# Optimization experiments

Measured on AMD Instinct MI355X. Metric: run time of the kernel, lower is better.

## Reference

```python
import jax, jax.numpy as jnp
import numpy as np

# Block sizes (DGL message-flow-graph / sampled blocks)
NS0, ND0, NE0 = 300000, 50000, 800000   # block0: 2-hop frontier -> 1-hop frontier
NS1, ND1, NE1 = 50000, 8192, 131072     # block1: 1-hop frontier -> seed nodes


def _graph_conv(x, src, dst, ew, W, b, n_src, n_dst, weight_first):
    """DGL GraphConv with norm='both' and edge_weight.

    x: [n_src, d_in] source-node features; (src, dst): edge endpoints;
    ew: [E] edge weights. Degrees are UNWEIGHTED (copy of DGL semantics),
    clamped to >= 1. Weight applied before aggregation iff d_in > d_out.
    """
    ones_e = jnp.ones_like(ew)
    out_deg = jnp.clip(jax.ops.segment_sum(ones_e, src, num_segments=n_src), 1.0, None)
    h = x * (out_deg ** -0.5)[:, None]
    if weight_first:
        h = h @ W
    # gather-weight-scatter: m_v = sum_{e: e->v} ew_e * h_{src_e}
    msg = jax.ops.segment_sum(ew[:, None] * h[src], dst, num_segments=n_dst)
    in_deg = jnp.clip(jax.ops.segment_sum(ones_e, dst, num_segments=n_dst), 1.0, None)
    msg = msg * (in_deg ** -0.5)[:, None]
    if not weight_first:
        msg = msg @ W
    return msg + b


def setup_inputs() -> dict:
    key = jax.random.key(0)
    ks = jax.random.split(key, 12)
    in_f, hid_f, out_f = 256, 128, 128
    return {
        "x": jax.random.normal(ks[0], (NS0, in_f), dtype=jnp.float32),
        "src0": jax.random.randint(ks[1], (NE0,), 0, NS0, dtype=jnp.int64 if jax.config.jax_enable_x64 else jnp.int32).astype(jnp.int32),
        "dst0": jax.random.randint(ks[2], (NE0,), 0, ND0).astype(jnp.int32),
        "ew0": jax.random.normal(ks[3], (NE0,), dtype=jnp.float32),
        "src1": jax.random.randint(ks[4], (NE1,), 0, NS1).astype(jnp.int32),
        "dst1": jax.random.randint(ks[5], (NE1,), 0, ND1).astype(jnp.int32),
        "ew1": jax.random.normal(ks[6], (NE1,), dtype=jnp.float32),
        "W1": jax.random.normal(ks[7], (in_f, hid_f), dtype=jnp.float32) * 0.05,
        "b1": jax.random.normal(ks[8], (hid_f,), dtype=jnp.float32) * 0.05,
        "W2": jax.random.normal(ks[9], (hid_f, out_f), dtype=jnp.float32) * 0.05,
        "b2": jax.random.normal(ks[10], (out_f,), dtype=jnp.float32) * 0.05,
    }


def reference(x, src0, dst0, ew0, src1, dst1, ew1, W1, b1, W2, b2):
    # layer 1: in(256) > hidden(128) -> weight applied before aggregation
    h = jax.nn.relu(_graph_conv(x, src0, dst0, ew0, W1, b1, NS0, ND0, weight_first=True))
    # layer 2: hidden(128) <= out(128) -> aggregate then weight
    out = jax.nn.relu(_graph_conv(h, src1, dst1, ew1, W2, b2, NS1, ND1, weight_first=False))
    return out  # [ND1, out_f]
```

## Files before the change

### kernel.cpp

```cpp
#include <hip/hip_runtime.h>

#define NS0 300000
#define ND0 50000
#define NE0 800000
#define NS1 50000
#define ND1 8192
#define NE1 131072
#define IN_F 256
#define HID_F 128
#define SLOTS 64
#define NTILE (NS0 / 16)
#define GEMM_GRID 2048

typedef __attribute__((ext_vector_type(8))) _Float16 half8_t;
typedef __attribute__((ext_vector_type(4))) _Float16 half4_t;
typedef __attribute__((ext_vector_type(4))) float f32x4;

#define OFF_OUTDEG0I 0
#define OFF_OUTDEG1I 300000
#define OFF_CNT0     350000
#define OFF_CNT1     400000
#define ZERO_WORDS   408192
#define OFF_EDGE0    408192
#define OFF_EDGE1    6808192
#define OFF_H1       7856768
#define OFF_W1T      14256768
#define OFF_G        14273152

__global__ __launch_bounds__(256) void k_zero(int4* __restrict__ p, int n4) {
  int i = blockIdx.x * 256 + threadIdx.x;
  int s = gridDim.x * 256;
  for (; i < n4; i += s) p[i] = make_int4(0, 0, 0, 0);
}

__global__ __launch_bounds__(256) void k_prep(
    const float* __restrict__ W1, _Float16* __restrict__ w1t) {
  int i = blockIdx.x * 256 + threadIdx.x;
  int s = gridDim.x * 256;
  for (; i < IN_F * HID_F; i += s) {
    int k = i >> 7, n = i & 127;
    w1t[n * 256 + k] = (_Float16)W1[i];
  }
}

__global__ __launch_bounds__(256) void k_build(
    const int* __restrict__ src0, const int* __restrict__ dst0,
    const float* __restrict__ ew0, int* __restrict__ outdeg0,
    int* __restrict__ cnt0, int2* __restrict__ edge0,
    const int* __restrict__ src1, const int* __restrict__ dst1,
    const float* __restrict__ ew1, int* __restrict__ outdeg1,
    int* __restrict__ cnt1, int2* __restrict__ edge1) {
  int tid = blockIdx.x * blockDim.x + threadIdx.x;
  int stride = gridDim.x * blockDim.x;
  for (int i = tid; i < NE0; i += stride) {
    int s = src0[i];
    int d = dst0[i];
    float w = ew0[i];
    atomicAdd(&outdeg0[s], 1);
    int slot = atomicAdd(&cnt0[d], 1);
    if (slot < SLOTS) edge0[d * SLOTS + slot] = make_int2(s, __float_as_int(w));
  }
  for (int i = tid; i < NE1; i += stride) {
    int s = src1[i];
    int d = dst1[i];
    float w = ew1[i];
    atomicAdd(&outdeg1[s], 1);
    int slot = atomicAdd(&cnt1[d], 1);
    if (slot < SLOTS) edge1[d * SLOTS + slot] = make_int2(s, __float_as_int(w));
  }
}

#define LDB(p, o) (*reinterpret_cast<const half8_t*>((p) + (o)))
__global__ __launch_bounds__(256) void k_gemm1(
    const float* __restrict__ x, const int* __restrict__ outdeg0,
    const _Float16* __restrict__ w1t, _Float16* __restrict__ g) {
  __shared__ __align__(16) _Float16 ldsA[2][16 * 256];
  __shared__ _Float16 ldsT[4][16 * 40];
  const int tid = threadIdx.x;
  const int wv = tid >> 6;
  const int lane = tid & 63;
  const int m = lane & 15;
  const int grp = lane >> 4;
  _Float16* tp = ldsT[wv];

  const _Float16* wb0 = w1t + (size_t)(32 * wv + m) * 256 + grp * 8;
  const _Float16* wb1 = wb0 + 16 * 256;
  const half8_t b00 = LDB(wb0, 0),   b01 = LDB(wb0, 32),  b02 = LDB(wb0, 64),
                b03 = LDB(wb0, 96),  b04 = LDB(wb0, 128), b05 = LDB(wb0, 160),
                b06 = LDB(wb0, 192), b07 = LDB(wb0, 224);
  const half8_t b10 = LDB(wb1, 0),   b11 = LDB(wb1, 32),  b12 = LDB(wb1, 64),
                b13 = LDB(wb1, 96),  b14 = LDB(wb1, 128), b15 = LDB(wb1, 160),
                b16 = LDB(wb1, 192), b17 = LDB(wb1, 224);

  const int skb = lane >> 3;
  const int sgrp = (lane >> 1) & 3;
  const int sjh = lane & 1;
  const int row_r = lane >> 2;
  const int q_r   = lane & 3;

  const int bid = blockIdx.x;
  float4 pv[4];
  float psc[4];

  {
    const float* tb = x + (size_t)bid * 4096;
#pragma unroll
    for (int r = 0; r < 4; ++r) {
      const int mr = wv + 4 * r;
      const float4 v = *reinterpret_cast<const float4*>(tb + tid * 4 + r * 1024);
      const float s = rsqrtf(fmaxf((float)outdeg0[bid * 16 + mr], 1.0f));
      half4_t h;
      h[0] = (_Float16)(v.x * s); h[1] = (_Float16)(v.y * s);
      h[2] = (_Float16)(v.z * s); h[3] = (_Float16)(v.w * s);
      const int idx = skb * 64 + sgrp * 16 + mr;
      const int S = idx ^ skb ^ sgrp;
      *reinterpret_cast<half4_t*>(
          reinterpret_cast<char*>(&ldsA[0][0]) + S * 16 + sjh * 8) = h;
    }
  }
  __syncthreads();

  int cur = 0;
  for (int tile = bid; tile < NTILE; tile += GEMM_GRID) {
    const int nxt = tile + GEMM_GRID;
    if (nxt < NTILE) {
      const float* tb = x + (size_t)nxt * 4096;
#pragma unroll
      for (int r = 0; r < 4; ++r) {
        pv[r] = *reinterpret_cast<const float4*>(tb + tid * 4 + r * 1024);
        psc[r] = rsqrtf(fmaxf((float)outdeg0[nxt * 16 + wv + 4 * r], 1.0f));
      }
    }
    {
      const char* A = reinterpret_cast<const char*>(&ldsA[cur][0]);
      f32x4 acc0 = {0.f, 0.f, 0.f, 0.f};
      f32x4 acc1 = {0.f, 0.f, 0.f, 0.f};
#define STEP(KB, B0, B1)                                                       \
  {                                                                            \
    const int Sr = ((KB * 64 + lane) ^ KB ^ grp);                              \
    const half8_t af = *reinterpret_cast<const half8_t*>(A + Sr * 16);         \
    acc0 = __builtin_amdgcn_mfma_f32_16x16x32_f16(af, B0, acc0, 0, 0, 0);      \
    acc1 = __builtin_amdgcn_mfma_f32_16x16x32_f16(af, B1, acc1, 0, 0, 0);      \
  }
      STEP(0, b00, b10)
      STEP(1, b01, b11)
      STEP(2, b02, b12)
      STEP(3, b03, b13)
      STEP(4, b04, b14)
      STEP(5, b05, b15)
      STEP(6, b06, b16)
      STEP(7, b07, b17)
#undef STEP
#pragma unroll
      for (int r = 0; r < 4; ++r) {
        tp[(4 * grp + r) * 40 + m]      = (_Float16)acc0[r];
        tp[(4 * grp + r) * 40 + 16 + m] = (_Float16)acc1[r];
      }
      const half8_t ov =
          *reinterpret_cast<const half8_t*>(tp + row_r * 40 + q_r * 8);
      *reinterpret_cast<half8_t*>(
          g + (size_t)(tile * 16 + row_r) * 128 + 32 * wv + q_r * 8) = ov;
    }
    if (nxt < NTILE) {
      char* B = reinterpret_cast<char*>(&ldsA[cur ^ 1][0]);
#pragma unroll
      for (int r = 0; r < 4; ++r) {
        const int mr = wv + 4 * r;
        half4_t h;
        h[0] = (_Float16)(pv[r].x * psc[r]); h[1] = (_Float16)(pv[r].y * psc[r]);
        h[2] = (_Float16)(pv[r].z * psc[r]); h[3] = (_Float16)(pv[r].w * psc[r]);
        const int idx = skb * 64 + sgrp * 16 + mr;
        const int S = idx ^ skb ^ sgrp;
        *reinterpret_cast<half4_t*>(B + S * 16 + sjh * 8) = h;
      }
    }
    __syncthreads();
    cur ^= 1;
  }
}

__global__ __launch_bounds__(256) void k_gather1(
    const _Float16* __restrict__ g, const int* __restrict__ cnt,
    const int2* __restrict__ edge, const int* __restrict__ outdeg1,
    const float* __restrict__ b1, float* __restrict__ h1) {
  const int w = (blockIdx.x * 256 + threadIdx.x) >> 6;
  const int lane = threadIdx.x & 63;
  const int gp = lane >> 4;
  const int sl = lane & 15;
  if (w >= ND0) return;
  const int deg = min(cnt[w], SLOTS);
  const int2* ep = edge + (size_t)w * SLOTS;
  float acc[8] = {0.f, 0.f, 0.f, 0.f, 0.f, 0.f, 0.f, 0.f};
  for (int e = 0; e < deg; e += 4) {
    const int idx = e + gp;
    int2 p = make_int2(0, 0);
    if (idx < deg) p = ep[idx];
    const float c = __int_as_float(p.y);
    const half8_t v =
        *reinterpret_cast<const half8_t*>(g + (size_t)p.x * 128 + sl * 8);
#pragma unroll
    for (int j = 0; j < 8; ++j) acc[j] = fmaf(c, (float)v[j], acc[j]);
  }
#pragma unroll
  for (int j = 0; j < 8; ++j) {
    acc[j] += __shfl_xor(acc[j], 16, 64);
    acc[j] += __shfl_xor(acc[j], 32, 64);
  }
  if (gp == 0) {
    const float sc = rsqrtf(fmaxf((float)deg, 1.0f));
    const float s1 = rsqrtf(fmaxf((float)outdeg1[w], 1.0f));
    const float4 bv0 = *reinterpret_cast<const float4*>(b1 + sl * 8);
    const float4 bv1 = *reinterpret_cast<const float4*>(b1 + sl * 8 + 4);
    float4 o0, o1;
    o0.x = fmaxf(fmaf(acc[0], sc, bv0.x), 0.0f) * s1;
    o0.y = fmaxf(fmaf(acc[1], sc, bv0.y), 0.0f) * s1;
    o0.z = fmaxf(fmaf(acc[2], sc, bv0.z), 0.0f) * s1;
    o0.w = fmaxf(fmaf(acc[3], sc, bv0.w), 0.0f) * s1;
    o1.x = fmaxf(fmaf(acc[4], sc, bv1.x), 0.0f) * s1;
    o1.y = fmaxf(fmaf(acc[5], sc, bv1.y), 0.0f) * s1;
    o1.z = fmaxf(fmaf(acc[6], sc, bv1.z), 0.0f) * s1;
    o1.w = fmaxf(fmaf(acc[7], sc, bv1.w), 0.0f) * s1;
    float* hr = h1 + (size_t)w * 128 + sl * 8;
    *reinterpret_cast<float4*>(hr) = o0;
    *reinterpret_cast<float4*>(hr + 4) = o1;
  }
}

#define FMA2(acc, c, v)        \
  acc.x = fmaf(c, v.x, acc.x); \
  acc.y = fmaf(c, v.y, acc.y);

__global__ __launch_bounds__(256) void k_layer2(
    const float* __restrict__ h1, const int* __restrict__ cnt,
    const int2* __restrict__ edge, const float* __restrict__ W2,
    const float* __restrict__ b2, float* __restrict__ out) {
  __shared__ float arow[8][HID_F];
  const int t = blockIdx.x;
  const int wv = threadIdx.x >> 6;
  const int lane = threadIdx.x & 63;

#pragma unroll
  for (int rr = 0; rr < 2; ++rr) {
    const int row = t * 8 + wv * 2 + rr;
    const int deg = min(cnt[row], SLOTS);
    const int2* ep = edge + (size_t)row * SLOTS;
    float2 acc = make_float2(0.f, 0.f);
    int e = 0;
    for (; e + 4 <= deg; e += 4) {
      int4 q0 = *reinterpret_cast<const int4*>(ep + e);
      int4 q1 = *reinterpret_cast<const int4*>(ep + e + 2);
      float2 v0 = *reinterpret_cast<const float2*>(h1 + (size_t)q0.x * HID_F + lane * 2);
      float2 v1 = *reinterpret_cast<const float2*>(h1 + (size_t)q0.z * HID_F + lane * 2);
      float2 v2 = *reinterpret_cast<const float2*>(h1 + (size_t)q1.x * HID_F + lane * 2);
      float2 v3 = *reinterpret_cast<const float2*>(h1 + (size_t)q1.z * HID_F + lane * 2);
      FMA2(acc, __int_as_float(q0.y), v0);
      FMA2(acc, __int_as_float(q0.w), v1);
      FMA2(acc, __int_as_float(q1.y), v2);
      FMA2(acc, __int_as_float(q1.w), v3);
    }
    for (; e < deg; ++e) {
      int2 p = ep[e];
      float2 v = *reinterpret_cast<const float2*>(h1 + (size_t)p.x * HID_F + lane * 2);
      FMA2(acc, __int_as_float(p.y), v);
    }
    const float sc = rsqrtf(fmaxf((float)deg, 1.0f));
    *reinterpret_cast<float2*>(&arow[wv * 2 + rr][lane * 2]) =
        make_float2(acc.x * sc, acc.y * sc);
  }
  __syncthreads();

  const int j = threadIdx.x & 127;
  const int rg = threadIdx.x >> 7;
  float a0 = 0.f, a1 = 0.f, a2 = 0.f, a3 = 0.f;
  const float* wj = W2 + j;
#pragma unroll 8
  for (int k = 0; k < HID_F; ++k) {
    const float wvv = wj[(size_t)k * 128];
    a0 = fmaf(arow[rg * 4 + 0][k], wvv, a0);
    a1 = fmaf(arow[rg * 4 + 1][k], wvv, a1);
    a2 = fmaf(arow[rg * 4 + 2][k], wvv, a2);
    a3 = fmaf(arow[rg * 4 + 3][k], wvv, a3);
  }
  const float bj = b2[j];
  const int row0 = t * 8 + rg * 4;
  out[(size_t)(row0 + 0) * 128 + j] = fmaxf(a0 + bj, 0.0f);
  out[(size_t)(row0 + 1) * 128 + j] = fmaxf(a1 + bj, 0.0f);
  out[(size_t)(row0 + 2) * 128 + j] = fmaxf(a2 + bj, 0.0f);
  out[(size_t)(row0 + 3) * 128 + j] = fmaxf(a3 + bj, 0.0f);
}

extern "C" void kernel_launch(void* const* d_in, const int* in_sizes, int n_in,
                              void* d_out, int out_size, void* d_ws, size_t ws_size,
                              hipStream_t stream) {
  const float* x    = (const float*)d_in[0];
  const int*   src0 = (const int*)d_in[1];
  const int*   dst0 = (const int*)d_in[2];
  const float* ew0  = (const float*)d_in[3];
  const int*   src1 = (const int*)d_in[4];
  const int*   dst1 = (const int*)d_in[5];
  const float* ew1  = (const float*)d_in[6];
  const float* W1   = (const float*)d_in[7];
  const float* b1   = (const float*)d_in[8];
  const float* W2   = (const float*)d_in[9];
  const float* b2   = (const float*)d_in[10];
  float* out = (float*)d_out;

  int*   wsi = (int*)d_ws;
  float* wsf = (float*)d_ws;
  int* outdeg0 = wsi + OFF_OUTDEG0I;
  int* outdeg1 = wsi + OFF_OUTDEG1I;
  int* cnt0    = wsi + OFF_CNT0;
  int* cnt1    = wsi + OFF_CNT1;
  int2* edge0  = (int2*)(wsi + OFF_EDGE0);
  int2* edge1  = (int2*)(wsi + OFF_EDGE1);
  float* h1    = wsf + OFF_H1;
  _Float16* w1t = (_Float16*)(wsi + OFF_W1T);
  _Float16* g   = (_Float16*)(wsi + OFF_G);

  k_zero<<<128, 256, 0, stream>>>((int4*)d_ws, ZERO_WORDS / 4);
  k_prep<<<32, 256, 0, stream>>>(W1, w1t);
  k_build<<<1024, 256, 0, stream>>>(src0, dst0, ew0, outdeg0, cnt0, edge0,
                                    src1, dst1, ew1, outdeg1, cnt1, edge1);
  k_gemm1<<<GEMM_GRID, 256, 0, stream>>>(x, outdeg0, w1t, g);
  k_gather1<<<(ND0 * 64) / 256, 256, 0, stream>>>(g, cnt0, edge0, outdeg1, b1, h1);
  k_layer2<<<ND1 / 8, 256, 0, stream>>>(h1, cnt1, edge1, W2, b2, out);
}
```

Before: 240.3 us.

## Overlap edge-list build with layer-1 GEMM by moving out-degree scaling into gather

Removes the GEMM's dependence on out-degree by applying the source normalisation per edge in the gather, instead of scaling x rows before the matmul. With that dependence gone, the edge build and the GEMM run as disjoint block ranges of one launch so their work overlaps. The zero-fill and weight-transpose kernels are merged into one init kernel to cut launches. In exchange the gather does an extra random outdeg0 read and rsqrt per edge, and the build blocks compete with GEMM blocks for CUs.

New measurement: 235.7 us. About the same (-1.9%).

```diff
diff --git a/kernel.cpp b/kernel.cpp
--- a/kernel.cpp
+++ b/kernel.cpp
@@ -11,6 +11,7 @@
 #define SLOTS 64
 #define NTILE (NS0 / 16)
 #define GEMM_GRID 2048
+#define BUILD_GRID 512
 
 typedef __attribute__((ext_vector_type(8))) _Float16 half8_t;
 typedef __attribute__((ext_vector_type(4))) _Float16 half4_t;
@@ -27,55 +28,56 @@
 #define OFF_W1T      14256768
 #define OFF_G        14273152
 
-__global__ __launch_bounds__(256) void k_zero(int4* __restrict__ p, int n4) {
-  int i = blockIdx.x * 256 + threadIdx.x;
-  int s = gridDim.x * 256;
-  for (; i < n4; i += s) p[i] = make_int4(0, 0, 0, 0);
-}
-
-__global__ __launch_bounds__(256) void k_prep(
-    const float* __restrict__ W1, _Float16* __restrict__ w1t) {
-  int i = blockIdx.x * 256 + threadIdx.x;
-  int s = gridDim.x * 256;
-  for (; i < IN_F * HID_F; i += s) {
-    int k = i >> 7, n = i & 127;
-    w1t[n * 256 + k] = (_Float16)W1[i];
-  }
-}
-
-__global__ __launch_bounds__(256) void k_build(
+__global__ __launch_bounds__(256) void k_init(
+    int4* __restrict__ p, const float* __restrict__ W1,
+    _Float16* __restrict__ w1t) {
+  if (blockIdx.x < 128) {
+    int i = blockIdx.x * 256 + threadIdx.x;
+    for (; i < ZERO_WORDS / 4; i += 128 * 256) p[i] = make_int4(0, 0, 0, 0);
+  } else {
+    int i = (blockIdx.x - 128) * 256 + threadIdx.x;
+    for (; i < IN_F * HID_F; i += 32 * 256) {
+      int k = i >> 7, n = i & 127;
+      w1t[n * 256 + k] = (_Float16)W1[i];
+    }
+  }
+}
+
+#define LDB(p, o) (*reinterpret_cast<const half8_t*>((p) + (o)))
+__global__ __launch_bounds__(256) void k_gemm_build(
+    const float* __restrict__ x, const _Float16* __restrict__ w1t,
+    _Float16* __restrict__ g,
     const int* __restrict__ src0, const int* __restrict__ dst0,
     const float* __restrict__ ew0, int* __restrict__ outdeg0,
     int* __restrict__ cnt0, int2* __restrict__ edge0,
     const int* __restrict__ src1, const int* __restrict__ dst1,
     const float* __restrict__ ew1, int* __restrict__ outdeg1,
     int* __restrict__ cnt1, int2* __restrict__ edge1) {
-  int tid = blockIdx.x * blockDim.x + threadIdx.x;
-  int stride = gridDim.x * blockDim.x;
-  for (int i = tid; i < NE0; i += stride) {
-    int s = src0[i];
-    int d = dst0[i];
-    float w = ew0[i];
-    atomicAdd(&outdeg0[s], 1);
-    int slot = atomicAdd(&cnt0[d], 1);
-    if (slot < SLOTS) edge0[d * SLOTS + slot] = make_int2(s, __float_as_int(w));
-  }
-  for (int i = tid; i < NE1; i += stride) {
-    int s = src1[i];
-    int d = dst1[i];
-    float w = ew1[i];
-    atomicAdd(&outdeg1[s], 1);
-    int slot = atomicAdd(&cnt1[d], 1);
-    if (slot < SLOTS) edge1[d * SLOTS + slot] = make_int2(s, __float_as_int(w));
-  }
-}
-
-#define LDB(p, o) (*reinterpret_cast<const half8_t*>((p) + (o)))
-__global__ __launch_bounds__(256) void k_gemm1(
-    const float* __restrict__ x, const int* __restrict__ outdeg0,
-    const _Float16* __restrict__ w1t, _Float16* __restrict__ g) {
   __shared__ __align__(16) _Float16 ldsA[2][16 * 256];
   __shared__ _Float16 ldsT[4][16 * 40];
+
+  if (blockIdx.x >= GEMM_GRID) {
+    int tid = (blockIdx.x - GEMM_GRID) * 256 + threadIdx.x;
+    int stride = BUILD_GRID * 256;
+    for (int i = tid; i < NE0; i += stride) {
+      int s = src0[i];
+      int d = dst0[i];
+      float w = ew0[i];
+      atomicAdd(&outdeg0[s], 1);
+      int slot = atomicAdd(&cnt0[d], 1);
+      if (slot < SLOTS) edge0[d * SLOTS + slot] = make_int2(s, __float_as_int(w));
+    }
+    for (int i = tid; i < NE1; i += stride) {
+      int s = src1[i];
+      int d = dst1[i];
+      float w = ew1[i];
+      atomicAdd(&outdeg1[s], 1);
+      int slot = atomicAdd(&cnt1[d], 1);
+      if (slot < SLOTS) edge1[d * SLOTS + slot] = make_int2(s, __float_as_int(w));
+    }
+    return;
+  }
+
   const int tid = threadIdx.x;
   const int wv = tid >> 6;
   const int lane = tid & 63;
@@ -100,7 +102,6 @@
 
   const int bid = blockIdx.x;
   float4 pv[4];
-  float psc[4];
 
   {
     const float* tb = x + (size_t)bid * 4096;
@@ -108,10 +109,9 @@
     for (int r = 0; r < 4; ++r) {
       const int mr = wv + 4 * r;
       const float4 v = *reinterpret_cast<const float4*>(tb + tid * 4 + r * 1024);
-      const float s = rsqrtf(fmaxf((float)outdeg0[bid * 16 + mr], 1.0f));
       half4_t h;
-      h[0] = (_Float16)(v.x * s); h[1] = (_Float16)(v.y * s);
-      h[2] = (_Float16)(v.z * s); h[3] = (_Float16)(v.w * s);
+      h[0] = (_Float16)v.x; h[1] = (_Float16)v.y;
+      h[2] = (_Float16)v.z; h[3] = (_Float16)v.w;
       const int idx = skb * 64 + sgrp * 16 + mr;
       const int S = idx ^ skb ^ sgrp;
       *reinterpret_cast<half4_t*>(
@@ -126,10 +126,8 @@
     if (nxt < NTILE) {
       const float* tb = x + (size_t)nxt * 4096;
 #pragma unroll
-      for (int r = 0; r < 4; ++r) {
+      for (int r = 0; r < 4; ++r)
         pv[r] = *reinterpret_cast<const float4*>(tb + tid * 4 + r * 1024);
-        psc[r] = rsqrtf(fmaxf((float)outdeg0[nxt * 16 + wv + 4 * r], 1.0f));
-      }
     }
     {
       const char* A = reinterpret_cast<const char*>(&ldsA[cur][0]);
@@ -167,8 +165,8 @@
       for (int r = 0; r < 4; ++r) {
         const int mr = wv + 4 * r;
         half4_t h;
-        h[0] = (_Float16)(pv[r].x * psc[r]); h[1] = (_Float16)(pv[r].y * psc[r]);
-        h[2] = (_Float16)(pv[r].z * psc[r]); h[3] = (_Float16)(pv[r].w * psc[r]);
+        h[0] = (_Float16)pv[r].x; h[1] = (_Float16)pv[r].y;
+        h[2] = (_Float16)pv[r].z; h[3] = (_Float16)pv[r].w;
         const int idx = skb * 64 + sgrp * 16 + mr;
         const int S = idx ^ skb ^ sgrp;
         *reinterpret_cast<half4_t*>(B + S * 16 + sjh * 8) = h;
@@ -181,8 +179,9 @@
 
 __global__ __launch_bounds__(256) void k_gather1(
     const _Float16* __restrict__ g, const int* __restrict__ cnt,
-    const int2* __restrict__ edge, const int* __restrict__ outdeg1,
-    const float* __restrict__ b1, float* __restrict__ h1) {
+    const int2* __restrict__ edge, const int* __restrict__ outdeg0,
+    const int* __restrict__ outdeg1, const float* __restrict__ b1,
+    float* __restrict__ h1) {
   const int w = (blockIdx.x * 256 + threadIdx.x) >> 6;
   const int lane = threadIdx.x & 63;
   const int gp = lane >> 4;
@@ -194,8 +193,11 @@
   for (int e = 0; e < deg; e += 4) {
     const int idx = e + gp;
     int2 p = make_int2(0, 0);
-    if (idx < deg) p = ep[idx];
-    const float c = __int_as_float(p.y);
+    float c = 0.f;
+    if (idx < deg) {
+      p = ep[idx];
+      c = __int_as_float(p.y) * rsqrtf(fmaxf((float)outdeg0[p.x], 1.0f));
+    }
     const half8_t v =
         *reinterpret_cast<const half8_t*>(g + (size_t)p.x * 128 + sl * 8);
 #pragma unroll
@@ -317,11 +319,11 @@
   _Float16* w1t = (_Float16*)(wsi + OFF_W1T);
   _Float16* g   = (_Float16*)(wsi + OFF_G);
 
-  k_zero<<<128, 256, 0, stream>>>((int4*)d_ws, ZERO_WORDS / 4);
-  k_prep<<<32, 256, 0, stream>>>(W1, w1t);
-  k_build<<<1024, 256, 0, stream>>>(src0, dst0, ew0, outdeg0, cnt0, edge0,
-                                    src1, dst1, ew1, outdeg1, cnt1, edge1);
-  k_gemm1<<<GEMM_GRID, 256, 0, stream>>>(x, outdeg0, w1t, g);
-  k_gather1<<<(ND0 * 64) / 256, 256, 0, stream>>>(g, cnt0, edge0, outdeg1, b1, h1);
+  k_init<<<160, 256, 0, stream>>>((int4*)d_ws, W1, w1t);
+  k_gemm_build<<<GEMM_GRID + BUILD_GRID, 256, 0, stream>>>(
+      x, w1t, g, src0, dst0, ew0, outdeg0, cnt0, edge0,
+      src1, dst1, ew1, outdeg1, cnt1, edge1);
+  k_gather1<<<(ND0 * 64) / 256, 256, 0, stream>>>(g, cnt0, edge0, outdeg0,
+                                                  outdeg1, b1, h1);
   k_layer2<<<ND1 / 8, 256, 0, stream>>>(h1, cnt1, edge1, W2, b2, out);
 }
```
